# Kernel tuning notes

Hardware: AMD Instinct MI355X
Metric: run time of the kernel (lower is better)

Reference implementation:

```python
import jax, jax.numpy as jnp
import numpy as np


def setup_inputs() -> dict:
    key = jax.random.key(0)
    k1, k2 = jax.random.split(key)
    n, d, num_classes = 262144, 128, 512
    inputs = jax.random.normal(k1, (n, d), dtype=jnp.float32)
    targets = jax.random.randint(k2, (n,), 0, num_classes)
    return {"inputs": inputs, "targets": targets, "num_classes": num_classes}


def reference(inputs, targets, num_classes):
    beta = 0.1
    eps = 1e-12  # torch F.normalize default eps (norm clamped to min eps)
    # L2-normalize features
    x = inputs / jnp.maximum(jnp.linalg.norm(inputs, axis=1, keepdims=True), eps)  # [n, d]

    # Per-class centers: mean of normalized features, then L2-normalize, detached.
    ones = jnp.ones((x.shape[0],), dtype=x.dtype)
    counts = jax.ops.segment_sum(ones, targets, num_segments=num_classes)          # [C]
    csum = jax.ops.segment_sum(x, targets, num_segments=num_classes)               # [C, d]
    cmean = csum / jnp.maximum(counts, 1.0)[:, None]
    centers = cmean / jnp.maximum(jnp.linalg.norm(cmean, axis=1, keepdims=True), eps)
    centers = jax.lax.stop_gradient(centers)  # .detach() in original

    # Numerator logit: center of own class dotted with own feature
    pos = jnp.sum(centers[targets] * x, axis=1) / beta                             # [n]
    # Denominator: sum of exp over all *present* classes (original only builds
    # centers for pids that appear in the batch)
    scores = jnp.exp(centers @ x.T / beta)                                         # [C, n]
    present = counts > 0
    denom = jnp.sum(jnp.where(present[:, None], scores, 0.0), axis=0)              # [n]
    return -jnp.mean(pos - jnp.log(denom))
```

## Files before the change

### kernel.cpp

```cpp
#include <hip/hip_runtime.h>
#include <stdint.h>

#define NROWS 262144
#define DDIM 128
#define NCLS 512
#define NHB 128
constexpr float INV_BETA = 10.0f;

typedef __bf16 v8bf __attribute__((ext_vector_type(8)));
typedef float v4f __attribute__((ext_vector_type(4)));

__device__ inline unsigned short f2bf(float f) {
    uint32_t u = __builtin_bit_cast(uint32_t, f);
    u += 0x7FFFu + ((u >> 16) & 1u);
    return (unsigned short)(u >> 16);
}
__device__ inline float bflo(uint32_t u) { return __builtin_bit_cast(float, u << 16); }
__device__ inline float bfhi(uint32_t u) { return __builtin_bit_cast(float, u & 0xFFFF0000u); }

__global__ __launch_bounds__(256) void k1_normalize(
    const float* __restrict__ in, unsigned short* __restrict__ xb) {
    int t = threadIdx.x;
    int w = t >> 6;
    int half = (t & 63) >> 5;
    int lane32 = t & 31;
    const int CH = NROWS / 2;
    for (int row = blockIdx.x * 8 + w * 2 + half; row < CH; row += 2048 * 8) {
        int rowB = row + CH;
        const float4 v0 = *reinterpret_cast<const float4*>(in + (size_t)row * DDIM + lane32 * 4);
        const float4 v1 = *reinterpret_cast<const float4*>(in + (size_t)rowB * DDIM + lane32 * 4);
        float s0 = v0.x * v0.x + v0.y * v0.y + v0.z * v0.z + v0.w * v0.w;
        float s1 = v1.x * v1.x + v1.y * v1.y + v1.z * v1.z + v1.w * v1.w;
#pragma unroll
        for (int off = 1; off < 32; off <<= 1) {
            s0 += __shfl_xor(s0, off);
            s1 += __shfl_xor(s1, off);
        }
        float i0 = rsqrtf(fmaxf(s0, 1e-24f));
        float i1 = rsqrtf(fmaxf(s1, 1e-24f));
        ushort4 o0, o1;
        o0.x = f2bf(v0.x * i0); o0.y = f2bf(v0.y * i0);
        o0.z = f2bf(v0.z * i0); o0.w = f2bf(v0.w * i0);
        o1.x = f2bf(v1.x * i1); o1.y = f2bf(v1.y * i1);
        o1.z = f2bf(v1.z * i1); o1.w = f2bf(v1.w * i1);
        *reinterpret_cast<ushort4*>(xb + (size_t)row * DDIM + lane32 * 4) = o0;
        *reinterpret_cast<ushort4*>(xb + (size_t)rowB * DDIM + lane32 * 4) = o1;
    }
}

__global__ __launch_bounds__(256) void k_hist(
    const int* __restrict__ tgt, int* __restrict__ counts, int* __restrict__ bh) {
    __shared__ int h[NCLS];
    int t = threadIdx.x;
    for (int i = t; i < NCLS; i += 256) h[i] = 0;
    __syncthreads();
    int base = blockIdx.x * (NROWS / NHB);
    for (int i = base + t; i < base + NROWS / NHB; i += 256)
        atomicAdd(&h[tgt[i]], 1);
    __syncthreads();
    for (int i = t; i < NCLS; i += 256) {
        int v = h[i];
        bh[blockIdx.x * NCLS + i] = v;
        if (v) atomicAdd(&counts[i], v);
    }
}

__global__ __launch_bounds__(512) void k_prefix(
    const int* __restrict__ counts, const int* __restrict__ bh,
    int* __restrict__ offs, int* __restrict__ base, float* __restrict__ nabsG) {
    __shared__ int sc[NCLS];
    __shared__ int za;
    int t = threadIdx.x;
    int c = counts[t];
    sc[t] = c;
    if (t == 0) za = 0;
    __syncthreads();
    for (int off = 1; off < NCLS; off <<= 1) {
        int v = (t >= off) ? sc[t - off] : 0;
        __syncthreads();
        sc[t] += v;
        __syncthreads();
    }
    int excl = sc[t] - c;
    offs[t] = excl;
    if (c == 0) atomicAdd(&za, 1);
    int run = excl;
    for (int b = 0; b < NHB; ++b) {
        base[b * NCLS + t] = run;
        run += bh[b * NCLS + t];
    }
    __syncthreads();
    if (t == 0) *nabsG = (float)za;
}

__global__ __launch_bounds__(256) void k_scatter(
    const int* __restrict__ tgt, const int* __restrict__ base, int* __restrict__ ridx) {
    __shared__ int cur[NCLS];
    int t = threadIdx.x;
    int b = blockIdx.x;
    cur[t] = base[b * NCLS + t];
    cur[t + 256] = base[b * NCLS + t + 256];
    __syncthreads();
    int r0 = b * (NROWS / NHB);
    for (int i = t; i < NROWS / NHB; i += 256) {
        int row = r0 + i;
        int c = tgt[row];
        int pos = atomicAdd(&cur[c], 1);
        ridx[pos] = row;
    }
}

__global__ __launch_bounds__(512) void k_centers(
    const unsigned short* __restrict__ xb, const int* __restrict__ ridx,
    const int* __restrict__ counts, const int* __restrict__ offs,
    unsigned short* __restrict__ cen) {
    __shared__ float2 sP[8][64];
    int t = threadIdx.x, w = t >> 6, l = t & 63;
    int cl = blockIdx.x;
    int cnt = counts[cl], start = offs[cl];
    const uint32_t* xb32 = (const uint32_t*)xb;
    float a0 = 0.0f, a1 = 0.0f;
    int per = (cnt + 7) >> 3;
    int lo = w * per, hi = min(cnt, lo + per);
    int i = lo;
    for (; i + 8 <= hi; i += 8) {
        int id[8]; uint32_t v[8];
#pragma unroll
        for (int j = 0; j < 8; ++j) id[j] = ridx[start + i + j];
#pragma unroll
        for (int j = 0; j < 8; ++j) v[j] = xb32[(size_t)id[j] * 64 + l];
#pragma unroll
        for (int j = 0; j < 8; ++j) { a0 += bflo(v[j]); a1 += bfhi(v[j]); }
    }
    for (; i < hi; ++i) {
        uint32_t v = xb32[(size_t)ridx[start + i] * 64 + l];
        a0 += bflo(v); a1 += bfhi(v);
    }
    sP[w][l] = make_float2(a0, a1);
    __syncthreads();
    if (w == 0) {
        float c0 = 0.0f, c1 = 0.0f;
#pragma unroll
        for (int q = 0; q < 8; ++q) { c0 += sP[q][l].x; c1 += sP[q][l].y; }
        float fc = fmaxf((float)cnt, 1.0f);
        c0 /= fc; c1 /= fc;
        float ss = c0 * c0 + c1 * c1;
        for (int off = 1; off < 64; off <<= 1) ss += __shfl_xor(ss, off);
        float inv = 1.0f / fmaxf(sqrtf(ss), 1e-12f);
        ushort2 o;
        o.x = f2bf(c0 * inv); o.y = f2bf(c1 * inv);
        *reinterpret_cast<ushort2*>(cen + (size_t)cl * DDIM + l * 2) = o;
    }
}

__global__ __launch_bounds__(512) void k4_loss(
    const unsigned short* __restrict__ xb, const unsigned short* __restrict__ cen,
    const int* __restrict__ tgt, const float* __restrict__ nabsG,
    float* __restrict__ out) {
    __shared__ char xL[2][16384];
    __shared__ float denP[8][64];
    __shared__ float posP[8][64];
    int t = threadIdx.x, w = t >> 6, l = t & 63;
    int lm = l & 15, lk = l >> 4;
    float nabs = *nabsG;

    v8bf afr[4][4];
#pragma unroll
    for (int m = 0; m < 4; ++m)
#pragma unroll
        for (int kc = 0; kc < 4; ++kc) {
            int row = w * 64 + m * 16 + lm;
            afr[m][kc] = *reinterpret_cast<const v8bf*>(cen + (size_t)row * DDIM + kc * 32 + lk * 8);
        }

    int block0 = blockIdx.x * 1024;
    int c0 = t * 2;
    int srow = c0 >> 4;
    int sw = (srow & 7) << 4;
    int dst0 = srow * 256 + (((c0 & 15) * 16) ^ sw);
    int dst1 = srow * 256 + ((((c0 & 15) + 1) * 16) ^ sw);
    const char* xbB = (const char*)xb;

    uint4 r0 = *(const uint4*)(xbB + (size_t)block0 * 256 + c0 * 16);
    uint4 r1 = *(const uint4*)(xbB + (size_t)block0 * 256 + c0 * 16 + 16);
    *(uint4*)(xL[0] + dst0) = r0;
    *(uint4*)(xL[0] + dst1) = r1;
    float lossAcc = 0.0f;
    __syncthreads();

    for (int tile = 0; tile < 16; ++tile) {
        int cur = tile & 1;
        int gbase = block0 + tile * 64;
        if (tile < 15) {
            const char* src = xbB + (size_t)(gbase + 64) * 256;
            r0 = *(const uint4*)(src + c0 * 16);
            r1 = *(const uint4*)(src + c0 * 16 + 16);
        }
        int ts[4];
#pragma unroll
        for (int n = 0; n < 4; ++n) ts[n] = tgt[gbase + n * 16 + lm];

        v4f acc[4][4];
        v4f zero = {0.0f, 0.0f, 0.0f, 0.0f};
#pragma unroll
        for (int m = 0; m < 4; ++m)
#pragma unroll
            for (int n = 0; n < 4; ++n) acc[m][n] = zero;

#pragma unroll
        for (int kc = 0; kc < 4; ++kc) {
            int kb = kc * 64 + lk * 16;
            v8bf b[4];
#pragma unroll
            for (int n = 0; n < 4; ++n) {
                int row = n * 16 + lm;
                b[n] = *reinterpret_cast<const v8bf*>(xL[cur] + row * 256 + (kb ^ ((row & 7) << 4)));
            }
#pragma unroll
            for (int m = 0; m < 4; ++m)
#pragma unroll
                for (int n = 0; n < 4; ++n)
                    acc[m][n] = __builtin_amdgcn_mfma_f32_16x16x32_bf16(afr[m][kc], b[n], acc[m][n], 0, 0, 0);
        }

#pragma unroll
        for (int n = 0; n < 4; ++n) {
            float se = 0.0f, sp = 0.0f;
#pragma unroll
            for (int m = 0; m < 4; ++m) {
#pragma unroll
                for (int r = 0; r < 4; ++r) {
                    int cls = w * 64 + m * 16 + lk * 4 + r;
                    float logit = acc[m][n][r] * INV_BETA;
                    se += __expf(logit);
                    if (cls == ts[n]) sp = logit;
                }
            }
            se += __shfl_xor(se, 16); se += __shfl_xor(se, 32);
            sp += __shfl_xor(sp, 16); sp += __shfl_xor(sp, 32);
            if (l < 16) { denP[w][n * 16 + lm] = se; posP[w][n * 16 + lm] = sp; }
        }
        __syncthreads();
        if (tile < 15) {
            *(uint4*)(xL[1 - cur] + dst0) = r0;
            *(uint4*)(xL[1 - cur] + dst1) = r1;
        }
        if (w == 0) {
            float den = 0.0f, pos = 0.0f;
#pragma unroll
            for (int q = 0; q < 8; ++q) { den += denP[q][l]; pos += posP[q][l]; }
            lossAcc += __logf(den - nabs) - pos;
        }
        __syncthreads();
    }
    if (w == 0) {
        for (int off = 1; off < 64; off <<= 1) lossAcc += __shfl_xor(lossAcc, off);
        if (l == 0) atomicAdd(out, lossAcc * (1.0f / NROWS));
    }
}

extern "C" void kernel_launch(void* const* d_in, const int* in_sizes, int n_in,
                              void* d_out, int out_size, void* d_ws, size_t ws_size,
                              hipStream_t stream) {
    const float* in = (const float*)d_in[0];
    const int* tgt = (const int*)d_in[1];
    float* out = (float*)d_out;
    char* ws = (char*)d_ws;
    unsigned short* xb = (unsigned short*)(ws);
    int* counts = (int*)(ws + 67108864);
    int* offs = (int*)(ws + 67110912);
    float* nabsG = (float*)(ws + 67112960);
    unsigned short* cen = (unsigned short*)(ws + 67115264);
    int* ridx = (int*)(ws + 67246336);
    int* bh = (int*)(ws + 68294912);
    int* base = (int*)(ws + 68557056);

    hipMemsetAsync(counts, 0, 2048, stream);
    hipMemsetAsync(out, 0, sizeof(float), stream);
    hipLaunchKernelGGL(k1_normalize, dim3(2048), dim3(256), 0, stream, in, xb);
    hipLaunchKernelGGL(k_hist, dim3(NHB), dim3(256), 0, stream, tgt, counts, bh);
    hipLaunchKernelGGL(k_prefix, dim3(1), dim3(512), 0, stream, counts, bh, offs, base, nabsG);
    hipLaunchKernelGGL(k_scatter, dim3(NHB), dim3(256), 0, stream, tgt, base, ridx);
    hipLaunchKernelGGL(k_centers, dim3(NCLS), dim3(512), 0, stream, xb, ridx, counts, offs, cen);
    hipLaunchKernelGGL(k4_loss, dim3(256), dim3(512), 0, stream, xb, cen, tgt, nabsG, out);
}
```

Measured before the change: 133.6 us.

## Widen loss tiles, preload targets, drop memsets, and unroll normalize rows

The loss kernel now stages 128-row tiles (8 iterations instead of 16) in dynamic LDS with 64-byte loads per thread. It preloads all targets into LDS and spreads the final log reduction across all waves. The normalize kernel handles four rows per thread instead of two, for more memory-level parallelism. Counts are now summed in the prefix kernel from per-block histograms, which also zeroes the output, removing two memsets and the global atomics. The costs are more LDS per block (about 78KB), which can lower occupancy, and a serial 128-step sum in the single-block prefix kernel.

After: 138.8 us. 1.04x slower.

```diff
diff --git a/kernel.cpp b/kernel.cpp
--- a/kernel.cpp
+++ b/kernel.cpp
@@ -24,32 +24,34 @@
     int w = t >> 6;
     int half = (t & 63) >> 5;
     int lane32 = t & 31;
-    const int CH = NROWS / 2;
+    const int CH = NROWS / 4;
     for (int row = blockIdx.x * 8 + w * 2 + half; row < CH; row += 2048 * 8) {
-        int rowB = row + CH;
-        const float4 v0 = *reinterpret_cast<const float4*>(in + (size_t)row * DDIM + lane32 * 4);
-        const float4 v1 = *reinterpret_cast<const float4*>(in + (size_t)rowB * DDIM + lane32 * 4);
-        float s0 = v0.x * v0.x + v0.y * v0.y + v0.z * v0.z + v0.w * v0.w;
-        float s1 = v1.x * v1.x + v1.y * v1.y + v1.z * v1.z + v1.w * v1.w;
+        float4 v[4];
+#pragma unroll
+        for (int j = 0; j < 4; ++j)
+            v[j] = *reinterpret_cast<const float4*>(in + (size_t)(row + j * CH) * DDIM + lane32 * 4);
+        float s[4];
+#pragma unroll
+        for (int j = 0; j < 4; ++j)
+            s[j] = v[j].x * v[j].x + v[j].y * v[j].y + v[j].z * v[j].z + v[j].w * v[j].w;
 #pragma unroll
         for (int off = 1; off < 32; off <<= 1) {
-            s0 += __shfl_xor(s0, off);
-            s1 += __shfl_xor(s1, off);
-        }
-        float i0 = rsqrtf(fmaxf(s0, 1e-24f));
-        float i1 = rsqrtf(fmaxf(s1, 1e-24f));
-        ushort4 o0, o1;
-        o0.x = f2bf(v0.x * i0); o0.y = f2bf(v0.y * i0);
-        o0.z = f2bf(v0.z * i0); o0.w = f2bf(v0.w * i0);
-        o1.x = f2bf(v1.x * i1); o1.y = f2bf(v1.y * i1);
-        o1.z = f2bf(v1.z * i1); o1.w = f2bf(v1.w * i1);
-        *reinterpret_cast<ushort4*>(xb + (size_t)row * DDIM + lane32 * 4) = o0;
-        *reinterpret_cast<ushort4*>(xb + (size_t)rowB * DDIM + lane32 * 4) = o1;
+#pragma unroll
+            for (int j = 0; j < 4; ++j) s[j] += __shfl_xor(s[j], off);
+        }
+#pragma unroll
+        for (int j = 0; j < 4; ++j) {
+            float iv = rsqrtf(fmaxf(s[j], 1e-24f));
+            ushort4 o;
+            o.x = f2bf(v[j].x * iv); o.y = f2bf(v[j].y * iv);
+            o.z = f2bf(v[j].z * iv); o.w = f2bf(v[j].w * iv);
+            *reinterpret_cast<ushort4*>(xb + (size_t)(row + j * CH) * DDIM + lane32 * 4) = o;
+        }
     }
 }
 
 __global__ __launch_bounds__(256) void k_hist(
-    const int* __restrict__ tgt, int* __restrict__ counts, int* __restrict__ bh) {
+    const int* __restrict__ tgt, int* __restrict__ bh) {
     __shared__ int h[NCLS];
     int t = threadIdx.x;
     for (int i = t; i < NCLS; i += 256) h[i] = 0;
@@ -58,21 +60,20 @@
     for (int i = base + t; i < base + NROWS / NHB; i += 256)
         atomicAdd(&h[tgt[i]], 1);
     __syncthreads();
-    for (int i = t; i < NCLS; i += 256) {
-        int v = h[i];
-        bh[blockIdx.x * NCLS + i] = v;
-        if (v) atomicAdd(&counts[i], v);
-    }
+    for (int i = t; i < NCLS; i += 256)
+        bh[blockIdx.x * NCLS + i] = h[i];
 }
 
 __global__ __launch_bounds__(512) void k_prefix(
-    const int* __restrict__ counts, const int* __restrict__ bh,
-    int* __restrict__ offs, int* __restrict__ base, float* __restrict__ nabsG) {
+    const int* __restrict__ bh, int* __restrict__ counts, int* __restrict__ offs,
+    int* __restrict__ base, float* __restrict__ nabsG, float* __restrict__ out) {
     __shared__ int sc[NCLS];
     __shared__ int za;
     int t = threadIdx.x;
-    int c = counts[t];
-    sc[t] = c;
+    int cnt = 0;
+    for (int b = 0; b < NHB; ++b) cnt += bh[b * NCLS + t];
+    counts[t] = cnt;
+    sc[t] = cnt;
     if (t == 0) za = 0;
     __syncthreads();
     for (int off = 1; off < NCLS; off <<= 1) {
@@ -81,16 +82,16 @@
         sc[t] += v;
         __syncthreads();
     }
-    int excl = sc[t] - c;
+    int excl = sc[t] - cnt;
     offs[t] = excl;
-    if (c == 0) atomicAdd(&za, 1);
+    if (cnt == 0) atomicAdd(&za, 1);
     int run = excl;
     for (int b = 0; b < NHB; ++b) {
         base[b * NCLS + t] = run;
         run += bh[b * NCLS + t];
     }
     __syncthreads();
-    if (t == 0) *nabsG = (float)za;
+    if (t == 0) { *nabsG = (float)za; *out = 0.0f; }
 }
 
 __global__ __launch_bounds__(256) void k_scatter(
@@ -157,9 +158,13 @@
     const unsigned short* __restrict__ xb, const unsigned short* __restrict__ cen,
     const int* __restrict__ tgt, const float* __restrict__ nabsG,
     float* __restrict__ out) {
-    __shared__ char xL[2][16384];
-    __shared__ float denP[8][64];
-    __shared__ float posP[8][64];
+    extern __shared__ char lds[];
+    char* xL0 = lds;
+    char* xL1 = lds + 32768;
+    float* denP = (float*)(lds + 65536);
+    float* posP = (float*)(lds + 69632);
+    int* tgtL = (int*)(lds + 73728);
+    float* wsum = (float*)(lds + 77824);
     int t = threadIdx.x, w = t >> 6, l = t & 63;
     int lm = l & 15, lk = l >> 4;
     float nabs = *nabsG;
@@ -169,93 +174,107 @@
     for (int m = 0; m < 4; ++m)
 #pragma unroll
         for (int kc = 0; kc < 4; ++kc) {
-            int row = w * 64 + m * 16 + lm;
-            afr[m][kc] = *reinterpret_cast<const v8bf*>(cen + (size_t)row * DDIM + kc * 32 + lk * 8);
+            int arow = w * 64 + m * 16 + lm;
+            afr[m][kc] = *reinterpret_cast<const v8bf*>(cen + (size_t)arow * DDIM + kc * 32 + lk * 8);
         }
 
     int block0 = blockIdx.x * 1024;
-    int c0 = t * 2;
-    int srow = c0 >> 4;
+    tgtL[t] = tgt[block0 + t];
+    tgtL[t + 512] = tgt[block0 + t + 512];
+
+    int srow = t >> 2;
     int sw = (srow & 7) << 4;
-    int dst0 = srow * 256 + (((c0 & 15) * 16) ^ sw);
-    int dst1 = srow * 256 + ((((c0 & 15) + 1) * 16) ^ sw);
-    const char* xbB = (const char*)xb;
-
-    uint4 r0 = *(const uint4*)(xbB + (size_t)block0 * 256 + c0 * 16);
-    uint4 r1 = *(const uint4*)(xbB + (size_t)block0 * 256 + c0 * 16 + 16);
-    *(uint4*)(xL[0] + dst0) = r0;
-    *(uint4*)(xL[0] + dst1) = r1;
+    int cb = (t & 3) * 64;
+    int dst[4];
+#pragma unroll
+    for (int j = 0; j < 4; ++j) dst[j] = srow * 256 + ((cb + j * 16) ^ sw);
+    const char* xbB = (const char*)xb + (size_t)block0 * 256;
+
+    uint4 r[4];
+#pragma unroll
+    for (int j = 0; j < 4; ++j) r[j] = *(const uint4*)(xbB + t * 64 + j * 16);
+#pragma unroll
+    for (int j = 0; j < 4; ++j) *(uint4*)(xL0 + dst[j]) = r[j];
     float lossAcc = 0.0f;
     __syncthreads();
 
-    for (int tile = 0; tile < 16; ++tile) {
-        int cur = tile & 1;
-        int gbase = block0 + tile * 64;
-        if (tile < 15) {
-            const char* src = xbB + (size_t)(gbase + 64) * 256;
-            r0 = *(const uint4*)(src + c0 * 16);
-            r1 = *(const uint4*)(src + c0 * 16 + 16);
-        }
-        int ts[4];
-#pragma unroll
-        for (int n = 0; n < 4; ++n) ts[n] = tgt[gbase + n * 16 + lm];
-
-        v4f acc[4][4];
-        v4f zero = {0.0f, 0.0f, 0.0f, 0.0f};
-#pragma unroll
-        for (int m = 0; m < 4; ++m)
-#pragma unroll
-            for (int n = 0; n < 4; ++n) acc[m][n] = zero;
-
-#pragma unroll
-        for (int kc = 0; kc < 4; ++kc) {
-            int kb = kc * 64 + lk * 16;
-            v8bf b[4];
+    for (int tile = 0; tile < 8; ++tile) {
+        char* xc = (tile & 1) ? xL1 : xL0;
+        char* xn = (tile & 1) ? xL0 : xL1;
+        if (tile < 7) {
+            const char* src = xbB + (size_t)(tile + 1) * 32768 + t * 64;
+#pragma unroll
+            for (int j = 0; j < 4; ++j) r[j] = *(const uint4*)(src + j * 16);
+        }
+
+#pragma unroll
+        for (int h = 0; h < 2; ++h) {
+            v4f acc[4][4];
+            v4f zero = {0.0f, 0.0f, 0.0f, 0.0f};
+#pragma unroll
+            for (int m = 0; m < 4; ++m)
+#pragma unroll
+                for (int n = 0; n < 4; ++n) acc[m][n] = zero;
+
+#pragma unroll
+            for (int kc = 0; kc < 4; ++kc) {
+                int kb = kc * 64 + lk * 16;
+                v8bf b[4];
+#pragma unroll
+                for (int n = 0; n < 4; ++n) {
+                    int brow = h * 64 + n * 16 + lm;
+                    b[n] = *reinterpret_cast<const v8bf*>(xc + brow * 256 + (kb ^ ((brow & 7) << 4)));
+                }
+#pragma unroll
+                for (int m = 0; m < 4; ++m)
+#pragma unroll
+                    for (int n = 0; n < 4; ++n)
+                        acc[m][n] = __builtin_amdgcn_mfma_f32_16x16x32_bf16(afr[m][kc], b[n], acc[m][n], 0, 0, 0);
+            }
+
 #pragma unroll
             for (int n = 0; n < 4; ++n) {
-                int row = n * 16 + lm;
-                b[n] = *reinterpret_cast<const v8bf*>(xL[cur] + row * 256 + (kb ^ ((row & 7) << 4)));
+                int s = h * 64 + n * 16 + lm;
+                int ts = tgtL[tile * 128 + s];
+                float se = 0.0f, sp = 0.0f;
+#pragma unroll
+                for (int m = 0; m < 4; ++m) {
+#pragma unroll
+                    for (int rr = 0; rr < 4; ++rr) {
+                        int cls = w * 64 + m * 16 + lk * 4 + rr;
+                        float logit = acc[m][n][rr] * INV_BETA;
+                        se += __expf(logit);
+                        if (cls == ts) sp = logit;
+                    }
+                }
+                se += __shfl_xor(se, 16); se += __shfl_xor(se, 32);
+                sp += __shfl_xor(sp, 16); sp += __shfl_xor(sp, 32);
+                if (l < 16) { denP[w * 128 + s] = se; posP[w * 128 + s] = sp; }
             }
-#pragma unroll
-            for (int m = 0; m < 4; ++m)
-#pragma unroll
-                for (int n = 0; n < 4; ++n)
-                    acc[m][n] = __builtin_amdgcn_mfma_f32_16x16x32_bf16(afr[m][kc], b[n], acc[m][n], 0, 0, 0);
-        }
-
-#pragma unroll
-        for (int n = 0; n < 4; ++n) {
-            float se = 0.0f, sp = 0.0f;
-#pragma unroll
-            for (int m = 0; m < 4; ++m) {
-#pragma unroll
-                for (int r = 0; r < 4; ++r) {
-                    int cls = w * 64 + m * 16 + lk * 4 + r;
-                    float logit = acc[m][n][r] * INV_BETA;
-                    se += __expf(logit);
-                    if (cls == ts[n]) sp = logit;
-                }
-            }
-            se += __shfl_xor(se, 16); se += __shfl_xor(se, 32);
-            sp += __shfl_xor(sp, 16); sp += __shfl_xor(sp, 32);
-            if (l < 16) { denP[w][n * 16 + lm] = se; posP[w][n * 16 + lm] = sp; }
         }
         __syncthreads();
-        if (tile < 15) {
-            *(uint4*)(xL[1 - cur] + dst0) = r0;
-            *(uint4*)(xL[1 - cur] + dst1) = r1;
-        }
-        if (w == 0) {
+        if (tile < 7) {
+#pragma unroll
+            for (int j = 0; j < 4; ++j) *(uint4*)(xn + dst[j]) = r[j];
+        }
+        if (l < 16) {
+            int s = w * 16 + lm;
             float den = 0.0f, pos = 0.0f;
 #pragma unroll
-            for (int q = 0; q < 8; ++q) { den += denP[q][l]; pos += posP[q][l]; }
+            for (int q = 0; q < 8; ++q) { den += denP[q * 128 + s]; pos += posP[q * 128 + s]; }
             lossAcc += __logf(den - nabs) - pos;
         }
         __syncthreads();
     }
-    if (w == 0) {
-        for (int off = 1; off < 64; off <<= 1) lossAcc += __shfl_xor(lossAcc, off);
-        if (l == 0) atomicAdd(out, lossAcc * (1.0f / NROWS));
+#pragma unroll
+    for (int off = 1; off < 16; off <<= 1) lossAcc += __shfl_xor(lossAcc, off);
+    if (l == 0) wsum[w] = lossAcc;
+    __syncthreads();
+    if (t == 0) {
+        float s = 0.0f;
+#pragma unroll
+        for (int q = 0; q < 8; ++q) s += wsum[q];
+        atomicAdd(out, s * (1.0f / NROWS));
     }
 }
 
@@ -275,12 +294,13 @@
     int* bh = (int*)(ws + 68294912);
     int* base = (int*)(ws + 68557056);
 
-    hipMemsetAsync(counts, 0, 2048, stream);
-    hipMemsetAsync(out, 0, sizeof(float), stream);
+    (void)hipFuncSetAttribute((const void*)k4_loss,
+                              hipFuncAttributeMaxDynamicSharedMemorySize, 77856);
+
     hipLaunchKernelGGL(k1_normalize, dim3(2048), dim3(256), 0, stream, in, xb);
-    hipLaunchKernelGGL(k_hist, dim3(NHB), dim3(256), 0, stream, tgt, counts, bh);
-    hipLaunchKernelGGL(k_prefix, dim3(1), dim3(512), 0, stream, counts, bh, offs, base, nabsG);
+    hipLaunchKernelGGL(k_hist, dim3(NHB), dim3(256), 0, stream, tgt, bh);
+    hipLaunchKernelGGL(k_prefix, dim3(1), dim3(512), 0, stream, bh, counts, offs, base, nabsG, out);
     hipLaunchKernelGGL(k_scatter, dim3(NHB), dim3(256), 0, stream, tgt, base, ridx);
     hipLaunchKernelGGL(k_centers, dim3(NCLS), dim3(512), 0, stream, xb, ridx, counts, offs, cen);
-    hipLaunchKernelGGL(k4_loss, dim3(256), dim3(512), 0, stream, xb, cen, tgt, nabsG, out);
-}
+    hipLaunchKernelGGL(k4_loss, dim3(256), dim3(512), 77856, stream, xb, cen, tgt, nabsG, out);
+}
```
